# Optimization experiments

Measured on AMD Instinct MI355X. Metric: run time of the kernel, lower is better.

## Reference

```python
import jax, jax.numpy as jnp
import numpy as np

B = 131072
C = 1000

def setup_inputs() -> dict:
    key = jax.random.key(0)
    k1, k2, k3 = jax.random.split(key, 3)
    outputs = jax.random.normal(k1, (B, C), dtype=jnp.float32)
    targets = jax.random.randint(k2, (B,), 0, C)
    # penalty matrix in [1, 3): mimics dict penalties >= 1 for confused pairs
    penalty_matrix = 1.0 + 2.0 * jax.random.uniform(k3, (C, C), dtype=jnp.float32)
    return {"outputs": outputs, "targets": targets, "penalty_matrix": penalty_matrix}

def reference(outputs, targets, penalty_matrix):
    # per-sample cross entropy: -log_softmax(outputs)[i, targets[i]]
    logp = jax.nn.log_softmax(outputs, axis=-1)            # [B, C]
    base_losses = -jnp.take_along_axis(logp, targets[:, None], axis=-1)[:, 0]  # [B]
    predicted = jnp.argmax(outputs, axis=-1)               # [B]
    penalties = penalty_matrix[targets, predicted]         # [B], dense table = dict lookup
    return jnp.mean(base_losses * penalties)
```

## Files before the change

### kernel.cpp

```cpp
#include <hip/hip_runtime.h>


#define NCLASS   1000
#define NC4      250
#define BLK      256
#define WPB      4
#define NBLOCKS  2048

__global__ __launch_bounds__(BLK) void cal_rows(
    const float* __restrict__ outputs,
    const int*   __restrict__ targets,
    const float* __restrict__ penalty,
    float* __restrict__ partials,
    int B)
{
    const int lane  = threadIdx.x & 63;
    const int widx  = threadIdx.x >> 6;
    const int gwave = blockIdx.x * WPB + widx;
    const int nwave = gridDim.x * WPB;

    float acc = 0.0f;

    for (int row = gwave; row < B; row += nwave) {
        const float4* rp = reinterpret_cast<const float4*>(outputs + (size_t)row * NCLASS);
        const float NEG = -__builtin_inff();

        float4 v0 = rp[lane];
        float4 v1 = rp[lane + 64];
        float4 v2 = rp[lane + 128];
        float4 v3;
        const int c3 = lane + 192;
        if (c3 < NC4) v3 = rp[c3];
        else { v3.x = NEG; v3.y = NEG; v3.z = NEG; v3.w = NEG; }

        float mval = v0.x; int midx = 4 * lane;
        #define UPD(val, col) do { if ((val) > mval) { mval = (val); midx = (col); } } while (0)
        UPD(v0.y, 4*lane + 1); UPD(v0.z, 4*lane + 2); UPD(v0.w, 4*lane + 3);
        { int b = 4*(lane +  64); UPD(v1.x, b); UPD(v1.y, b+1); UPD(v1.z, b+2); UPD(v1.w, b+3); }
        { int b = 4*(lane + 128); UPD(v2.x, b); UPD(v2.y, b+1); UPD(v2.z, b+2); UPD(v2.w, b+3); }
        { int b = 4*(lane + 192); UPD(v3.x, b); UPD(v3.y, b+1); UPD(v3.z, b+2); UPD(v3.w, b+3); }
        #undef UPD

        #pragma unroll
        for (int off = 32; off > 0; off >>= 1) {
            float ov = __shfl_xor(mval, off, 64);
            int   oi = __shfl_xor(midx, off, 64);
            if (ov > mval || (ov == mval && oi < midx)) { mval = ov; midx = oi; }
        }

        float s;
        s  = __expf(v0.x - mval) + __expf(v0.y - mval) + __expf(v0.z - mval) + __expf(v0.w - mval);
        s += __expf(v1.x - mval) + __expf(v1.y - mval) + __expf(v1.z - mval) + __expf(v1.w - mval);
        s += __expf(v2.x - mval) + __expf(v2.y - mval) + __expf(v2.z - mval) + __expf(v2.w - mval);
        s += __expf(v3.x - mval) + __expf(v3.y - mval) + __expf(v3.z - mval) + __expf(v3.w - mval);
        #pragma unroll
        for (int off = 32; off > 0; off >>= 1) s += __shfl_xor(s, off, 64);

        const int t   = targets[row];
        const int c4t = t >> 2;
        const int lt  = c4t & 63;
        const int jt  = c4t >> 6;
        const int et  = t & 3;
        float4 vv = (jt == 0) ? v0 : (jt == 1) ? v1 : (jt == 2) ? v2 : v3;
        float  xe = (et == 0) ? vv.x : (et == 1) ? vv.y : (et == 2) ? vv.z : vv.w;
        float tval = __shfl(xe, lt, 64);

        if (lane == 0) {
            float pen = penalty[(size_t)t * NCLASS + midx];
            acc += (mval + __logf(s) - tval) * pen;
        }
    }

    __shared__ float wsum[WPB];
    if (lane == 0) wsum[widx] = acc;
    __syncthreads();
    if (threadIdx.x == 0)
        partials[blockIdx.x] = wsum[0] + wsum[1] + wsum[2] + wsum[3];
}

__global__ __launch_bounds__(256) void cal_final(
    const float* __restrict__ partials, int n, float* __restrict__ out, float invB)
{
    float s = 0.0f;
    for (int i = threadIdx.x; i < n; i += 256) s += partials[i];
    #pragma unroll
    for (int off = 32; off > 0; off >>= 1) s += __shfl_xor(s, off, 64);
    __shared__ float wsum[4];
    const int widx = threadIdx.x >> 6;
    const int lane = threadIdx.x & 63;
    if (lane == 0) wsum[widx] = s;
    __syncthreads();
    if (threadIdx.x == 0) out[0] = (wsum[0] + wsum[1] + wsum[2] + wsum[3]) * invB;
}

extern "C" void kernel_launch(void* const* d_in, const int* in_sizes, int n_in,
                              void* d_out, int out_size, void* d_ws, size_t ws_size,
                              hipStream_t stream)
{
    const float* outputs = (const float*)d_in[0];
    const int*   targets = (const int*)d_in[1];
    const float* penalty = (const float*)d_in[2];
    float* out = (float*)d_out;
    const int B = in_sizes[1];

    float* partials = (float*)d_ws;
    int grid = NBLOCKS;
    if (ws_size < (size_t)grid * sizeof(float))
        grid = (int)(ws_size / sizeof(float));

    cal_rows<<<grid, BLK, 0, stream>>>(outputs, targets, penalty, partials, B);
    cal_final<<<1, 256, 0, stream>>>(partials, grid, out, 1.0f / (float)B);
}
```

Measured before the change: 96.95 us.

## Assign contiguous row chunks per wave and prefetch next row during compute

```diff
diff --git a/kernel.cpp b/kernel.cpp
--- a/kernel.cpp
+++ b/kernel.cpp
@@ -5,70 +5,98 @@
 #define NC4      250
 #define BLK      256
 #define WPB      4
-#define NBLOCKS  2048
+#define RPW      16
+
+typedef float f32x4 __attribute__((ext_vector_type(4)));
+
+__device__ __forceinline__ void load_row(const float* __restrict__ outputs,
+                                         int row, int lane,
+                                         f32x4& v0, f32x4& v1, f32x4& v2, f32x4& v3)
+{
+    const f32x4* rp = reinterpret_cast<const f32x4*>(outputs + (size_t)row * NCLASS);
+    const float NEG = -__builtin_inff();
+    v0 = rp[lane];
+    v1 = rp[lane + 64];
+    v2 = rp[lane + 128];
+    if (lane + 192 < NC4) v3 = rp[lane + 192];
+    else { v3.x = NEG; v3.y = NEG; v3.z = NEG; v3.w = NEG; }
+}
+
+__device__ __forceinline__ float row_term(f32x4 v0, f32x4 v1, f32x4 v2, f32x4 v3,
+                                          int t, int lane,
+                                          const float* __restrict__ penalty)
+{
+    float mval = v0.x; int midx = 4 * lane;
+    #define UPD(val, col) do { if ((val) > mval) { mval = (val); midx = (col); } } while (0)
+    UPD(v0.y, 4*lane + 1); UPD(v0.z, 4*lane + 2); UPD(v0.w, 4*lane + 3);
+    { int b = 4*(lane +  64); UPD(v1.x, b); UPD(v1.y, b+1); UPD(v1.z, b+2); UPD(v1.w, b+3); }
+    { int b = 4*(lane + 128); UPD(v2.x, b); UPD(v2.y, b+1); UPD(v2.z, b+2); UPD(v2.w, b+3); }
+    { int b = 4*(lane + 192); UPD(v3.x, b); UPD(v3.y, b+1); UPD(v3.z, b+2); UPD(v3.w, b+3); }
+    #undef UPD
+
+    #pragma unroll
+    for (int off = 32; off > 0; off >>= 1) {
+        float ov = __shfl_xor(mval, off, 64);
+        int   oi = __shfl_xor(midx, off, 64);
+        if (ov > mval || (ov == mval && oi < midx)) { mval = ov; midx = oi; }
+    }
+
+    float s;
+    s  = __expf(v0.x - mval) + __expf(v0.y - mval) + __expf(v0.z - mval) + __expf(v0.w - mval);
+    s += __expf(v1.x - mval) + __expf(v1.y - mval) + __expf(v1.z - mval) + __expf(v1.w - mval);
+    s += __expf(v2.x - mval) + __expf(v2.y - mval) + __expf(v2.z - mval) + __expf(v2.w - mval);
+    s += __expf(v3.x - mval) + __expf(v3.y - mval) + __expf(v3.z - mval) + __expf(v3.w - mval);
+    #pragma unroll
+    for (int off = 32; off > 0; off >>= 1) s += __shfl_xor(s, off, 64);
+
+    const int c4t = t >> 2;
+    const int lt  = c4t & 63;
+    const int jt  = c4t >> 6;
+    const int et  = t & 3;
+    f32x4 vv = (jt == 0) ? v0 : (jt == 1) ? v1 : (jt == 2) ? v2 : v3;
+    float  xe = (et == 0) ? vv.x : (et == 1) ? vv.y : (et == 2) ? vv.z : vv.w;
+    float tval = __shfl(xe, lt, 64);
+
+    float term = 0.0f;
+    if (lane == 0) {
+        float pen = penalty[(size_t)t * NCLASS + midx];
+        term = (mval + __logf(s) - tval) * pen;
+    }
+    return term;
+}
 
 __global__ __launch_bounds__(BLK) void cal_rows(
     const float* __restrict__ outputs,
     const int*   __restrict__ targets,
     const float* __restrict__ penalty,
-    float* __restrict__ partials,
+    float*       __restrict__ partials,
     int B)
 {
     const int lane  = threadIdx.x & 63;
     const int widx  = threadIdx.x >> 6;
     const int gwave = blockIdx.x * WPB + widx;
-    const int nwave = gridDim.x * WPB;
+
+    const int r0   = gwave * RPW;
+    const int rend = min(r0 + RPW, B);
 
     float acc = 0.0f;
 
-    for (int row = gwave; row < B; row += nwave) {
-        const float4* rp = reinterpret_cast<const float4*>(outputs + (size_t)row * NCLASS);
-        const float NEG = -__builtin_inff();
+    if (r0 < rend) {
+        f32x4 a0, a1, a2, a3;
+        load_row(outputs, r0, lane, a0, a1, a2, a3);
+        int t_cur = targets[r0];
 
-        float4 v0 = rp[lane];
-        float4 v1 = rp[lane + 64];
-        float4 v2 = rp[lane + 128];
-        float4 v3;
-        const int c3 = lane + 192;
-        if (c3 < NC4) v3 = rp[c3];
-        else { v3.x = NEG; v3.y = NEG; v3.z = NEG; v3.w = NEG; }
+        int row = r0;
+        for (; row + 1 < rend; ++row) {
+            f32x4 b0, b1, b2, b3;
+            load_row(outputs, row + 1, lane, b0, b1, b2, b3);
+            int t_nxt = targets[row + 1];
 
-        float mval = v0.x; int midx = 4 * lane;
-        #define UPD(val, col) do { if ((val) > mval) { mval = (val); midx = (col); } } while (0)
-        UPD(v0.y, 4*lane + 1); UPD(v0.z, 4*lane + 2); UPD(v0.w, 4*lane + 3);
-        { int b = 4*(lane +  64); UPD(v1.x, b); UPD(v1.y, b+1); UPD(v1.z, b+2); UPD(v1.w, b+3); }
-        { int b = 4*(lane + 128); UPD(v2.x, b); UPD(v2.y, b+1); UPD(v2.z, b+2); UPD(v2.w, b+3); }
-        { int b = 4*(lane + 192); UPD(v3.x, b); UPD(v3.y, b+1); UPD(v3.z, b+2); UPD(v3.w, b+3); }
-        #undef UPD
+            acc += row_term(a0, a1, a2, a3, t_cur, lane, penalty);
 
-        #pragma unroll
-        for (int off = 32; off > 0; off >>= 1) {
-            float ov = __shfl_xor(mval, off, 64);
-            int   oi = __shfl_xor(midx, off, 64);
-            if (ov > mval || (ov == mval && oi < midx)) { mval = ov; midx = oi; }
+            a0 = b0; a1 = b1; a2 = b2; a3 = b3; t_cur = t_nxt;
         }
-
-        float s;
-        s  = __expf(v0.x - mval) + __expf(v0.y - mval) + __expf(v0.z - mval) + __expf(v0.w - mval);
-        s += __expf(v1.x - mval) + __expf(v1.y - mval) + __expf(v1.z - mval) + __expf(v1.w - mval);
-        s += __expf(v2.x - mval) + __expf(v2.y - mval) + __expf(v2.z - mval) + __expf(v2.w - mval);
-        s += __expf(v3.x - mval) + __expf(v3.y - mval) + __expf(v3.z - mval) + __expf(v3.w - mval);
-        #pragma unroll
-        for (int off = 32; off > 0; off >>= 1) s += __shfl_xor(s, off, 64);
-
-        const int t   = targets[row];
-        const int c4t = t >> 2;
-        const int lt  = c4t & 63;
-        const int jt  = c4t >> 6;
-        const int et  = t & 3;
-        float4 vv = (jt == 0) ? v0 : (jt == 1) ? v1 : (jt == 2) ? v2 : v3;
-        float  xe = (et == 0) ? vv.x : (et == 1) ? vv.y : (et == 2) ? vv.z : vv.w;
-        float tval = __shfl(xe, lt, 64);
-
-        if (lane == 0) {
-            float pen = penalty[(size_t)t * NCLASS + midx];
-            acc += (mval + __logf(s) - tval) * pen;
-        }
+        acc += row_term(a0, a1, a2, a3, t_cur, lane, penalty);
     }
 
     __shared__ float wsum[WPB];
@@ -103,8 +131,8 @@
     float* out = (float*)d_out;
     const int B = in_sizes[1];
 
+    int grid = (B + WPB * RPW - 1) / (WPB * RPW);
     float* partials = (float*)d_ws;
-    int grid = NBLOCKS;
     if (ws_size < (size_t)grid * sizeof(float))
         grid = (int)(ws_size / sizeof(float));
 
```

Result: slower. 110.0 us (+13.4%).
